# Optimization experiments

Hardware: AMD Instinct MI355X
Metric: run time of the kernel (lower is better)

## Reference

```python
import jax, jax.numpy as jnp
import numpy as np

N = 100000
E = 1000000
NODE_DIM = 128
EDGE_DIM = 32
HID = 64
HIER = 32
NUM_CLASS = 10
NUM_LAYERS = 3
BN_EPS = 1e-5


def setup_inputs() -> dict:
    key = jax.random.key(0)
    ks = jax.random.split(key, 16)
    s = 0.05
    return {
        "x": jax.random.normal(ks[0], (N, NODE_DIM), jnp.float32),
        "e": jax.random.normal(ks[1], (E, EDGE_DIM), jnp.float32),
        "c": jax.random.normal(ks[2], (N, HIER), jnp.float32),
        "w_node": jax.random.normal(ks[3], (NODE_DIM, HID), jnp.float32) * s,
        "b_node": jnp.zeros((HID,), jnp.float32),
        "w_edge": jax.random.normal(ks[4], (EDGE_DIM, HID), jnp.float32) * s,
        "b_edge": jnp.zeros((HID,), jnp.float32),
        "w_out1": jax.random.normal(ks[5], (HIER + HID, 2 * HID), jnp.float32) * s,
        "b_out1": jnp.zeros((2 * HID,), jnp.float32),
        "bn_gamma": jnp.ones((2 * HID,), jnp.float32),
        "bn_beta": jnp.zeros((2 * HID,), jnp.float32),
        "prelu_a": jnp.asarray(0.25, jnp.float32),
        "w_out2": jax.random.normal(ks[6], (2 * HID, NUM_CLASS), jnp.float32) * s,
        "b_out2": jnp.zeros((NUM_CLASS,), jnp.float32),
        "edge_index": jax.random.randint(ks[7], (2, E), 0, N, jnp.int64),
    }


def reference(x, e, c, w_node, b_node, w_edge, b_edge, w_out1, b_out1,
              bn_gamma, bn_beta, prelu_a, w_out2, b_out2, edge_index):
    n = x.shape[0]
    h = x @ w_node + b_node                      # [N, HID]
    eh = e @ w_edge + b_edge                     # [E, HID]
    src, dst = edge_index[0], edge_index[1]
    loop = jnp.arange(n)
    # add_self_loops + zero self-loop edge_attr (done inside each GCN layer,
    # identical every layer so hoisted)
    src_f = jnp.concatenate([src, loop])
    dst_f = jnp.concatenate([dst, loop])
    e_f = jnp.concatenate([eh, jnp.zeros((n, eh.shape[1]), eh.dtype)], axis=0)
    deg = jax.ops.segment_sum(jnp.ones(dst_f.shape, x.dtype), dst_f, num_segments=n)
    dinv = deg ** -0.5                           # deg >= 1 thanks to self loops
    norm = (dinv[src_f] * dinv[dst_f])[:, None]  # [E+N, 1]
    h_sum = h
    for _ in range(NUM_LAYERS):
        msg = norm * (h[src_f] + e_f)            # gather + edge compute
        h = jax.ops.segment_sum(msg, dst_f, num_segments=n)  # scatter-add
        h = jax.nn.leaky_relu(h, 0.2)
        h_sum = h_sum + h                        # sum over h_list
    z = jnp.concatenate([h_sum, c], axis=-1) @ w_out1 + b_out1
    # BatchNorm1d (training-mode batch statistics, biased variance)
    mu = z.mean(axis=0)
    var = z.var(axis=0)
    z = (z - mu) / jnp.sqrt(var + BN_EPS) * bn_gamma + bn_beta
    z = jnp.where(z > 0, z, prelu_a * z)         # PReLU (single param)
    return z @ w_out2 + b_out2
```

## Files before the change

### kernel.cpp

```cpp
#include <hip/hip_runtime.h>
#include <math.h>

#define N_NODES 100000
#define N_EDGES 1000000
#define HID     64
#define HIER    32
#define NDIM    128
#define EDIM    32
#define K1      96
#define C1      128
#define NCLS    10
#define BN_EPS  1e-5f
#define SCAN_B  98
#define HTILES2 782
#define ZSTRIPS 6250

typedef __attribute__((ext_vector_type(8))) short short8;
typedef __attribute__((ext_vector_type(4))) float f32x4;

__device__ __forceinline__ unsigned pk_bf16(float a, float b) {
    unsigned ua = __float_as_uint(a);
    ua = (ua + 0x7FFFu + ((ua >> 16) & 1u)) >> 16;
    unsigned ub = __float_as_uint(b);
    ub = (ub + 0x7FFFu + ((ub >> 16) & 1u)) & 0xFFFF0000u;
    return ua | ub;
}
__device__ __forceinline__ float bf_lo(unsigned g) { return __uint_as_float(g << 16); }
__device__ __forceinline__ float bf_hi(unsigned g) { return __uint_as_float(g & 0xFFFF0000u); }
__device__ __forceinline__ short8 as_s8(uint4 u) {
    union { uint4 u; short8 s; } c; c.u = u; return c.s;
}


__global__ void k_count(const int* __restrict__ ei, int* __restrict__ cnt) {
    int i = blockIdx.x * blockDim.x + threadIdx.x;
    if (i < N_EDGES) atomicAdd(&cnt[ei[N_EDGES + i]], 1);
}

__global__ void k_scan1(const int* __restrict__ cnt, int* __restrict__ offs,
                        float* __restrict__ dinv, int* __restrict__ bsum) {
    __shared__ int buf[2][1024];
    int t = threadIdx.x, b = blockIdx.x;
    int i = b * 1024 + t;
    int v = (i < N_NODES) ? cnt[i] : 0;
    buf[0][t] = v; __syncthreads();
    int pi = 0;
    for (int off = 1; off < 1024; off <<= 1) {
        int x = buf[pi][t];
        if (t >= off) x += buf[pi][t - off];
        buf[pi ^ 1][t] = x; __syncthreads(); pi ^= 1;
    }
    int incl = buf[pi][t];
    if (i < N_NODES) {
        offs[i] = incl - v;
        dinv[i] = rsqrtf((float)(v + 1));
    }
    if (t == 1023) bsum[b] = incl;
}

__global__ void k_scan2(int* __restrict__ bsum, int nb) {
    __shared__ int buf[2][1024];
    int t = threadIdx.x;
    int v = (t < nb) ? bsum[t] : 0;
    buf[0][t] = v; __syncthreads();
    int pi = 0;
    for (int off = 1; off < 1024; off <<= 1) {
        int x = buf[pi][t];
        if (t >= off) x += buf[pi][t - off];
        buf[pi ^ 1][t] = x; __syncthreads(); pi ^= 1;
    }
    int incl = buf[pi][t];
    if (t < nb) bsum[t] = incl - v;
}

__global__ void k_scan3(const int* __restrict__ bsum, int* __restrict__ offs) {
    int b = blockIdx.x;
    int i = b * 1024 + threadIdx.x;
    if (i < N_NODES) offs[i] += bsum[b];
    if (i == 0) offs[N_NODES] = N_EDGES;
}

__global__ void k_fill(const int* __restrict__ ei, const int* __restrict__ offs,
                       int* __restrict__ cursor, const float* __restrict__ dinv,
                       uint2* __restrict__ epk) {
    int i = blockIdx.x * blockDim.x + threadIdx.x;
    if (i >= N_EDGES) return;
    int s = ei[i], d = ei[N_EDGES + i];
    int pos = offs[d] + atomicAdd(&cursor[d], 1);
    unsigned nhi = pk_bf16(dinv[s], 0.f) << 16;
    epk[pos] = make_uint2((unsigned)i | ((unsigned)(s & 0xFFF) << 20),
                          nhi | (unsigned)(s >> 12));
}


__global__ __launch_bounds__(256) void k_conv(const float4* __restrict__ e4,
                                              uint4* __restrict__ eb4) {
    int i = blockIdx.x * 256 + threadIdx.x;
    float4 a = e4[(size_t)2 * i];
    float4 b = e4[(size_t)2 * i + 1];
    uint4 pk;
    pk.x = pk_bf16(a.x, a.y); pk.y = pk_bf16(a.z, a.w);
    pk.z = pk_bf16(b.x, b.y); pk.w = pk_bf16(b.z, b.w);
    eb4[i] = pk;
}

__global__ __launch_bounds__(256) void k_conv2(const float4* __restrict__ c4,
                                               uint2* __restrict__ cb2) {
    int i = blockIdx.x * 256 + threadIdx.x;
    if (i >= N_NODES * 8) return;
    float4 a = c4[i];
    cb2[i] = make_uint2(pk_bf16(a.x, a.y), pk_bf16(a.z, a.w));
}

__global__ __launch_bounds__(256) void k_wpack(const float* __restrict__ w1,
                                               uint4* __restrict__ bpkg) {
    int i = blockIdx.x * 256 + threadIdx.x;
    if (i >= 12 * C1) return;
    int g = i >> 7, n = i & 127;
    uint4 r;
    r.x = pk_bf16(w1[(8 * g + 0) * C1 + n], w1[(8 * g + 1) * C1 + n]);
    r.y = pk_bf16(w1[(8 * g + 2) * C1 + n], w1[(8 * g + 3) * C1 + n]);
    r.z = pk_bf16(w1[(8 * g + 4) * C1 + n], w1[(8 * g + 5) * C1 + n]);
    r.w = pk_bf16(w1[(8 * g + 6) * C1 + n], w1[(8 * g + 7) * C1 + n]);
    bpkg[i] = r;
}


__global__ __launch_bounds__(256) void k_agg3(const unsigned* __restrict__ ebfu,
                                              const uint2* __restrict__ epk,
                                              const int* __restrict__ offs,
                                              const float* __restrict__ dinv,
                                              float* __restrict__ agg,
                                              float* __restrict__ wsumv) {
    int v = (blockIdx.x * 256 + threadIdx.x) >> 4;
    if (v >= N_NODES) return;
    int q = threadIdx.x & 15;
    int start = offs[v], end = offs[v + 1];
    float ax = 0.f, ay = 0.f, wacc = 0.f;
    for (int i = start; i < end; i += 4) {
        int i1 = i + 1, i2 = i + 2, i3 = i + 3;
        uint2 p0 = epk[i];
        uint2 p1 = (i1 < end) ? epk[i1] : make_uint2(0u, 0u);
        uint2 p2 = (i2 < end) ? epk[i2] : make_uint2(0u, 0u);
        uint2 p3 = (i3 < end) ? epk[i3] : make_uint2(0u, 0u);
        float n0 = bf_hi(p0.y), n1 = bf_hi(p1.y);
        float n2 = bf_hi(p2.y), n3 = bf_hi(p3.y);
        unsigned g0 = ebfu[(size_t)(p0.x & 0xFFFFFu) * 16 + q];
        unsigned g1 = ebfu[(size_t)(p1.x & 0xFFFFFu) * 16 + q];
        unsigned g2 = ebfu[(size_t)(p2.x & 0xFFFFFu) * 16 + q];
        unsigned g3 = ebfu[(size_t)(p3.x & 0xFFFFFu) * 16 + q];
        ax += n0 * bf_lo(g0) + n1 * bf_lo(g1) + n2 * bf_lo(g2) + n3 * bf_lo(g3);
        ay += n0 * bf_hi(g0) + n1 * bf_hi(g1) + n2 * bf_hi(g2) + n3 * bf_hi(g3);
        wacc += n0 + n1 + n2 + n3;
    }
    float dv = dinv[v];
    *(float2*)&agg[(size_t)v * EDIM + q * 2] = make_float2(dv * ax, dv * ay);
    if (q == 0) wsumv[v] = dv * wacc;
}


__global__ __launch_bounds__(256) void k_h0t2(const float* __restrict__ x,
                                              const float* __restrict__ w,
                                              const float* __restrict__ bias,
                                              unsigned* __restrict__ hbf) {
    __shared__ __align__(16) unsigned wpk[NDIM * 36];
    __shared__ float xt[128 * 33];
    for (int i = threadIdx.x; i < NDIM * 32; i += 256) {
        int k = i >> 5, j = i & 31;
        wpk[k * 36 + j] = pk_bf16(w[k * HID + 2 * j], w[k * HID + 2 * j + 1]);
    }
    int tid = threadIdx.x;
    int lane = tid & 63, wave = tid >> 6;
    int lr = lane >> 3, lc = lane & 7;
    int rbase = wave * 32 + lr * 4;
    int cbase = lc * 8;
    float bA[8];
    #pragma unroll
    for (int j = 0; j < 8; ++j) bA[j] = bias[cbase + j];
    for (int tile = blockIdx.x; tile < HTILES2; tile += gridDim.x) {
        int row0 = tile * 128;
        float acc[4][8];
        #pragma unroll
        for (int i = 0; i < 4; ++i)
            #pragma unroll
            for (int j = 0; j < 8; ++j) acc[i][j] = 0.f;
        for (int ch = 0; ch < 4; ++ch) {
            __syncthreads();
            #pragma unroll
            for (int p = 0; p < 4; ++p) {
                int idx = p * 256 + tid;
                int row = idx >> 3, kq = idx & 7;
                int gk = ch * 32 + kq * 4;
                float4 v = make_float4(0.f, 0.f, 0.f, 0.f);
                int gr = row0 + row;
                if (gr < N_NODES) v = *(const float4*)&x[(size_t)gr * NDIM + gk];
                float* d = &xt[row * 33 + kq * 4];
                d[0] = v.x; d[1] = v.y; d[2] = v.z; d[3] = v.w;
            }
            __syncthreads();
            for (int k = 0; k < 32; ++k) {
                float u[4];
                #pragma unroll
                for (int i = 0; i < 4; ++i) u[i] = xt[(rbase + i) * 33 + k];
                uint4 wp = *(const uint4*)&wpk[(ch * 32 + k) * 36 + lc * 4];
                float wv[8];
                wv[0] = bf_lo(wp.x); wv[1] = bf_hi(wp.x);
                wv[2] = bf_lo(wp.y); wv[3] = bf_hi(wp.y);
                wv[4] = bf_lo(wp.z); wv[5] = bf_hi(wp.z);
                wv[6] = bf_lo(wp.w); wv[7] = bf_hi(wp.w);
                #pragma unroll
                for (int i = 0; i < 4; ++i)
                    #pragma unroll
                    for (int j = 0; j < 8; ++j) acc[i][j] += u[i] * wv[j];
            }
        }
        #pragma unroll
        for (int i = 0; i < 4; ++i) {
            int gr = row0 + rbase + i;
            if (gr < N_NODES) {
                uint4 pk;
                pk.x = pk_bf16(acc[i][0] + bA[0], acc[i][1] + bA[1]);
                pk.y = pk_bf16(acc[i][2] + bA[2], acc[i][3] + bA[3]);
                pk.z = pk_bf16(acc[i][4] + bA[4], acc[i][5] + bA[5]);
                pk.w = pk_bf16(acc[i][6] + bA[6], acc[i][7] + bA[7]);
                *(uint4*)&hbf[(size_t)gr * 32 + (cbase >> 1)] = pk;
            }
        }
    }
}


__global__ __launch_bounds__(256) void k_se(const float* __restrict__ agg,
                                            const float* __restrict__ wsumv,
                                            const float* __restrict__ we,
                                            const float* __restrict__ be,
                                            unsigned* __restrict__ sebf) {
    int lane = threadIdx.x & 63, wid = threadIdx.x >> 6;
    float wreg[EDIM];
    #pragma unroll
    for (int k = 0; k < EDIM; ++k) wreg[k] = we[k * HID + lane];
    float bl = be[lane];
    for (int v = blockIdx.x * 4 + wid; v < N_NODES; v += gridDim.x * 4) {
        const float4* ar = (const float4*)(agg + (size_t)v * EDIM);
        float acc = wsumv[v] * bl;
        #pragma unroll
        for (int k4 = 0; k4 < EDIM / 4; ++k4) {
            float4 av = ar[k4];
            int k = k4 * 4;
            acc += av.x * wreg[k + 0] + av.y * wreg[k + 1] +
                   av.z * wreg[k + 2] + av.w * wreg[k + 3];
        }
        float partner = __shfl_xor(acc, 1);
        if ((lane & 1) == 0)
            sebf[(size_t)v * 32 + (lane >> 1)] = pk_bf16(acc, partner);
    }
}


__device__ __forceinline__ int dec_src(uint2 p) {
    return (int)(((p.y & 0xFFFFu) << 12) | (p.x >> 20));
}

__global__ __launch_bounds__(256) void k_layer4(const unsigned* __restrict__ hold,
                                                const unsigned* __restrict__ sebf,
                                                const uint2* __restrict__ epk,
                                                const int* __restrict__ offs,
                                                const float* __restrict__ dinv,
                                                unsigned* __restrict__ hnew) {
    int v = (blockIdx.x * 256 + threadIdx.x) >> 4;
    if (v >= N_NODES) return;
    int q = threadIdx.x & 15;
    int start = offs[v], end = offs[v + 1];
    float dv = dinv[v];
    size_t vp = (size_t)v * 16 + q;
    uint2 hv = ((const uint2*)hold)[vp];
    float a0 = dv * bf_lo(hv.x), a1 = dv * bf_hi(hv.x);
    float a2 = dv * bf_lo(hv.y), a3 = dv * bf_hi(hv.y);
    for (int i = start; i < end; i += 8) {
        int idx[8]; float nn[8]; uint2 gg[8];
        #pragma unroll
        for (int u = 0; u < 8; ++u) {
            int ii = i + u;
            uint2 p = (ii < end) ? epk[ii] : make_uint2(0u, 0u);
            idx[u] = dec_src(p);
            nn[u]  = bf_hi(p.y);
        }
        #pragma unroll
        for (int u = 0; u < 8; ++u) gg[u] = ((const uint2*)hold)[(size_t)idx[u] * 16 + q];
        #pragma unroll
        for (int u = 0; u < 8; ++u) {
            a0 += nn[u] * bf_lo(gg[u].x); a1 += nn[u] * bf_hi(gg[u].x);
            a2 += nn[u] * bf_lo(gg[u].y); a3 += nn[u] * bf_hi(gg[u].y);
        }
    }
    uint2 sv = ((const uint2*)sebf)[vp];
    float r0 = bf_lo(sv.x) + dv * a0;
    float r1 = bf_hi(sv.x) + dv * a1;
    float r2 = bf_lo(sv.y) + dv * a2;
    float r3 = bf_hi(sv.y) + dv * a3;
    r0 = (r0 > 0.f) ? r0 : 0.2f * r0;
    r1 = (r1 > 0.f) ? r1 : 0.2f * r1;
    r2 = (r2 > 0.f) ? r2 : 0.2f * r2;
    r3 = (r3 > 0.f) ? r3 : 0.2f * r3;
    ((uint2*)hnew)[vp] = make_uint2(pk_bf16(r0, r1), pk_bf16(r2, r3));
}

__global__ __launch_bounds__(256) void k_layer4s(const unsigned* __restrict__ hold,
                                                 const unsigned* __restrict__ hb0,
                                                 const unsigned* __restrict__ hb1,
                                                 const unsigned* __restrict__ sebf,
                                                 const uint2* __restrict__ epk,
                                                 const int* __restrict__ offs,
                                                 const float* __restrict__ dinv,
                                                 unsigned* __restrict__ hnew,
                                                 unsigned* __restrict__ hsbf) {
    int v = (blockIdx.x * 256 + threadIdx.x) >> 4;
    if (v >= N_NODES) return;
    int q = threadIdx.x & 15;
    int start = offs[v], end = offs[v + 1];
    float dv = dinv[v];
    size_t vp = (size_t)v * 16 + q;
    uint2 hv = ((const uint2*)hold)[vp];
    float a0 = dv * bf_lo(hv.x), a1 = dv * bf_hi(hv.x);
    float a2 = dv * bf_lo(hv.y), a3 = dv * bf_hi(hv.y);
    for (int i = start; i < end; i += 8) {
        int idx[8]; float nn[8]; uint2 gg[8];
        #pragma unroll
        for (int u = 0; u < 8; ++u) {
            int ii = i + u;
            uint2 p = (ii < end) ? epk[ii] : make_uint2(0u, 0u);
            idx[u] = dec_src(p);
            nn[u]  = bf_hi(p.y);
        }
        #pragma unroll
        for (int u = 0; u < 8; ++u) gg[u] = ((const uint2*)hold)[(size_t)idx[u] * 16 + q];
        #pragma unroll
        for (int u = 0; u < 8; ++u) {
            a0 += nn[u] * bf_lo(gg[u].x); a1 += nn[u] * bf_hi(gg[u].x);
            a2 += nn[u] * bf_lo(gg[u].y); a3 += nn[u] * bf_hi(gg[u].y);
        }
    }
    uint2 sv = ((const uint2*)sebf)[vp];
    float r0 = bf_lo(sv.x) + dv * a0;
    float r1 = bf_hi(sv.x) + dv * a1;
    float r2 = bf_lo(sv.y) + dv * a2;
    float r3 = bf_hi(sv.y) + dv * a3;
    r0 = (r0 > 0.f) ? r0 : 0.2f * r0;
    r1 = (r1 > 0.f) ? r1 : 0.2f * r1;
    r2 = (r2 > 0.f) ? r2 : 0.2f * r2;
    r3 = (r3 > 0.f) ? r3 : 0.2f * r3;
    ((uint2*)hnew)[vp] = make_uint2(pk_bf16(r0, r1), pk_bf16(r2, r3));
    uint2 g0 = ((const uint2*)hb0)[vp];
    uint2 g1 = ((const uint2*)hb1)[vp];
    float s0 = r0 + bf_lo(g0.x) + bf_lo(g1.x) + bf_lo(hv.x);
    float s1 = r1 + bf_hi(g0.x) + bf_hi(g1.x) + bf_hi(hv.x);
    float s2 = r2 + bf_lo(g0.y) + bf_lo(g1.y) + bf_lo(hv.y);
    float s3 = r3 + bf_hi(g0.y) + bf_hi(g1.y) + bf_hi(hv.y);
    ((uint2*)hsbf)[vp] = make_uint2(pk_bf16(s0, s1), pk_bf16(s2, s3));
}


__global__ __launch_bounds__(256) void k_zmfma(const unsigned* __restrict__ hsbf,
                                               const unsigned* __restrict__ cbf,
                                               const uint4* __restrict__ bpkg,
                                               const float* __restrict__ b1,
                                               unsigned* __restrict__ zbf,
                                               float* __restrict__ stats) {
    __shared__ float red[2][4][C1];
    int tid = threadIdx.x;
    int wave = tid >> 6, lane = tid & 63;
    int l15 = lane & 15, lg = lane >> 4;
    int strip = blockIdx.x * 4 + wave;
    float sN[8], qN[8];
    #pragma unroll
    for (int j = 0; j < 8; ++j) { sN[j] = 0.f; qN[j] = 0.f; }
    if (strip < ZSTRIPS) {
        int row = strip * 16 + l15;
        short8 A0 = as_s8(*(const uint4*)&hsbf[(size_t)row * 32 + lg * 4]);
        short8 A1 = as_s8(*(const uint4*)&hsbf[(size_t)row * 32 + 16 + lg * 4]);
        short8 A2 = as_s8(*(const uint4*)&cbf[(size_t)row * 16 + lg * 4]);
        int rb = strip * 16 + lg * 4;
        #pragma unroll
        for (int ct = 0; ct < 8; ++ct) {
            int n = ct * 16 + l15;
            short8 B0 = as_s8(bpkg[lg * C1 + n]);
            short8 B1 = as_s8(bpkg[(4 + lg) * C1 + n]);
            short8 B2 = as_s8(bpkg[(8 + lg) * C1 + n]);
            f32x4 acc = {0.f, 0.f, 0.f, 0.f};
            acc = __builtin_amdgcn_mfma_f32_16x16x32_bf16(A0, B0, acc, 0, 0, 0);
            acc = __builtin_amdgcn_mfma_f32_16x16x32_bf16(A1, B1, acc, 0, 0, 0);
            acc = __builtin_amdgcn_mfma_f32_16x16x32_bf16(A2, B2, acc, 0, 0, 0);
            float bias = b1[n];
            #pragma unroll
            for (int i = 0; i < 4; ++i) {
                float zz = acc[i] + bias;
                sN[ct] += zz; qN[ct] += zz * zz;
                float pz = __shfl_xor(zz, 1);
                if ((l15 & 1) == 0)
                    zbf[(size_t)(rb + i) * 64 + (n >> 1)] = pk_bf16(zz, pz);
            }
        }
    }
    #pragma unroll
    for (int j = 0; j < 8; ++j) {
        sN[j] += __shfl_xor(sN[j], 16); sN[j] += __shfl_xor(sN[j], 32);
        qN[j] += __shfl_xor(qN[j], 16); qN[j] += __shfl_xor(qN[j], 32);
    }
    if (lane < 16) {
        #pragma unroll
        for (int ct = 0; ct < 8; ++ct) {
            red[0][wave][ct * 16 + lane] = sN[ct];
            red[1][wave][ct * 16 + lane] = qN[ct];
        }
    }
    __syncthreads();
    if (tid < C1) {
        atomicAdd(&stats[tid],
                  red[0][0][tid] + red[0][1][tid] + red[0][2][tid] + red[0][3][tid]);
        atomicAdd(&stats[C1 + tid],
                  red[1][0][tid] + red[1][1][tid] + red[1][2][tid] + red[1][3][tid]);
    }
}

__global__ void k_ab(const float* __restrict__ stats, const float* __restrict__ gamma,
                     const float* __restrict__ beta, float* __restrict__ ab) {
    int t = threadIdx.x;
    if (t < C1) {
        float mu = stats[t] / (float)N_NODES;
        float var = stats[C1 + t] / (float)N_NODES - mu * mu;
        float inv = rsqrtf(var + BN_EPS);
        float a = gamma[t] * inv;
        ab[t] = a;
        ab[C1 + t] = beta[t] - mu * a;
    }
}


__global__ __launch_bounds__(256) void k_out3(const unsigned* __restrict__ zbf,
                                              const float* __restrict__ ab,
                                              const float* __restrict__ pa,
                                              const float* __restrict__ w2,
                                              const float* __restrict__ b2,
                                              float* __restrict__ out) {
    int v = blockIdx.x * 256 + threadIdx.x;
    if (v >= N_NODES) return;
    float alpha = pa[0];
    float acc[NCLS];
    #pragma unroll
    for (int j = 0; j < NCLS; ++j) acc[j] = b2[j];
    const uint4* zr = (const uint4*)(zbf + (size_t)v * 64);
    #pragma unroll
    for (int pk4 = 0; pk4 < 16; ++pk4) {
        uint4 g = zr[pk4];
        unsigned gw[4] = {g.x, g.y, g.z, g.w};
        #pragma unroll
        for (int w = 0; w < 4; ++w) {
            int d0 = pk4 * 8 + w * 2;
            float p0 = bf_lo(gw[w]) * ab[d0]     + ab[C1 + d0];
            float p1 = bf_hi(gw[w]) * ab[d0 + 1] + ab[C1 + d0 + 1];
            p0 = (p0 > 0.f) ? p0 : alpha * p0;
            p1 = (p1 > 0.f) ? p1 : alpha * p1;
            #pragma unroll
            for (int j = 0; j < NCLS; ++j)
                acc[j] += p0 * w2[d0 * NCLS + j] + p1 * w2[(d0 + 1) * NCLS + j];
        }
    }
    #pragma unroll
    for (int j = 0; j < NCLS; ++j) out[(size_t)v * NCLS + j] = acc[j];
}


extern "C" void kernel_launch(void* const* d_in, const int* in_sizes, int n_in,
                              void* d_out, int out_size, void* d_ws, size_t ws_size,
                              hipStream_t stream) {
    const float* x      = (const float*)d_in[0];
    const float* e      = (const float*)d_in[1];
    const float* c      = (const float*)d_in[2];
    const float* w_node = (const float*)d_in[3];
    const float* b_node = (const float*)d_in[4];
    const float* w_edge = (const float*)d_in[5];
    const float* b_edge = (const float*)d_in[6];
    const float* w_out1 = (const float*)d_in[7];
    const float* b_out1 = (const float*)d_in[8];
    const float* gamma  = (const float*)d_in[9];
    const float* beta   = (const float*)d_in[10];
    const float* pa     = (const float*)d_in[11];
    const float* w_out2 = (const float*)d_in[12];
    const float* b_out2 = (const float*)d_in[13];
    const int*   ei     = (const int*)d_in[14];
    float* out = (float*)d_out;

    char* wsb = (char*)d_ws;
    ushort*   ebf  = (ushort*)wsb;
    unsigned* sebf = (unsigned*)wsb;
    unsigned* zbf  = (unsigned*)(wsb + 12800000);
    size_t off = (64000000 + 255) & ~(size_t)255;
    auto alloc = [&](size_t bytes) {
        void* p = wsb + off;
        off = (off + bytes + 255) & ~(size_t)255;
        return p;
    };
    int*      cnt      = (int*)alloc(4ull * N_NODES);
    int*      offs     = (int*)alloc(4ull * (N_NODES + 1));
    float*    dinv     = (float*)alloc(4ull * N_NODES);
    int*      bsum     = (int*)alloc(4ull * 128);
    uint2*    epk      = (uint2*)alloc(8ull * N_EDGES);
    float*    agg      = (float*)alloc(4ull * N_NODES * EDIM);
    float*    wsumv    = (float*)alloc(4ull * N_NODES);
    float*    stats    = (float*)alloc(4ull * 256);
    float*    ab       = (float*)alloc(4ull * 256);
    unsigned* hb0      = (unsigned*)alloc(4ull * N_NODES * 32);
    unsigned* hb1      = (unsigned*)alloc(4ull * N_NODES * 32);
    unsigned* hb2      = (unsigned*)alloc(4ull * N_NODES * 32);
    unsigned* hb3      = (unsigned*)alloc(4ull * N_NODES * 32);
    unsigned* cbf      = (unsigned*)alloc(4ull * N_NODES * 16);
    uint4*    bpkg     = (uint4*)alloc(16ull * 12 * C1);
    unsigned* hsbf     = (unsigned*)agg;

    hipMemsetAsync(cnt, 0, 4ull * N_NODES, stream);
    hipMemsetAsync(stats, 0, 4ull * 256, stream);

    k_count<<<(N_EDGES + 255) / 256, 256, 0, stream>>>(ei, cnt);
    k_scan1<<<SCAN_B, 1024, 0, stream>>>(cnt, offs, dinv, bsum);
    k_scan2<<<1, 1024, 0, stream>>>(bsum, SCAN_B);
    k_scan3<<<SCAN_B, 1024, 0, stream>>>(bsum, offs);
    hipMemsetAsync(cnt, 0, 4ull * N_NODES, stream);
    k_fill<<<(N_EDGES + 255) / 256, 256, 0, stream>>>(ei, offs, cnt, dinv, epk);

    k_wpack<<<6, 256, 0, stream>>>(w_out1, bpkg);
    k_conv<<<15625, 256, 0, stream>>>((const float4*)e, (uint4*)ebf);
    k_agg3<<<N_NODES * 16 / 256, 256, 0, stream>>>((const unsigned*)ebf, epk,
                                                   offs, dinv, agg, wsumv);

    k_se<<<1280, 256, 0, stream>>>(agg, wsumv, w_edge, b_edge, sebf);
    k_conv2<<<(N_NODES * 8 + 255) / 256, 256, 0, stream>>>((const float4*)c, (uint2*)cbf);
    k_h0t2<<<HTILES2, 256, 0, stream>>>(x, w_node, b_node, hb0);

    k_layer4<<<N_NODES * 16 / 256, 256, 0, stream>>>(hb0, sebf, epk, offs, dinv, hb1);
    k_layer4<<<N_NODES * 16 / 256, 256, 0, stream>>>(hb1, sebf, epk, offs, dinv, hb2);
    k_layer4s<<<N_NODES * 16 / 256, 256, 0, stream>>>(hb2, hb0, hb1, sebf, epk, offs,
                                                      dinv, hb3, hsbf);

    k_zmfma<<<(ZSTRIPS + 3) / 4, 256, 0, stream>>>(hsbf, cbf, bpkg, b_out1, zbf, stats);
    k_ab<<<1, 128, 0, stream>>>(stats, gamma, beta, ab);
    k_out3<<<(N_NODES + 255) / 256, 256, 0, stream>>>(zbf, ab, pa, w_out2, b_out2, out);
}
```

Before: 432.0 us.

## Use MFMA for node projection and fuse conversion and cursor-init kernels

The scalar LDS-tiled x @ w_node kernel becomes a bf16 MFMA kernel that converts x to bf16 in registers and reads pre-packed weights built in an extended k_wpack. The e and c bf16 conversion kernels are merged into one launch. The scan now initializes the fill cursor with the offsets, which removes a memset and a load of offs per edge in k_fill. Rounding x to bf16 before the matmul adds precision error, and the launch count drops.

```diff
diff --git a/kernel.cpp b/kernel.cpp
--- a/kernel.cpp
+++ b/kernel.cpp
@@ -12,8 +12,9 @@
 #define NCLS    10
 #define BN_EPS  1e-5f
 #define SCAN_B  98
-#define HTILES2 782
 #define ZSTRIPS 6250
+#define CONV_E_BLOCKS 15625
+#define CONV_C_BLOCKS 3125
 
 typedef __attribute__((ext_vector_type(8))) short short8;
 typedef __attribute__((ext_vector_type(4))) float f32x4;
@@ -73,56 +74,75 @@
     if (t < nb) bsum[t] = incl - v;
 }
 
-__global__ void k_scan3(const int* __restrict__ bsum, int* __restrict__ offs) {
+__global__ void k_scan3(const int* __restrict__ bsum, int* __restrict__ offs,
+                        int* __restrict__ cursor) {
     int b = blockIdx.x;
     int i = b * 1024 + threadIdx.x;
-    if (i < N_NODES) offs[i] += bsum[b];
+    if (i < N_NODES) {
+        int v = offs[i] + bsum[b];
+        offs[i] = v;
+        cursor[i] = v;
+    }
     if (i == 0) offs[N_NODES] = N_EDGES;
 }
 
-__global__ void k_fill(const int* __restrict__ ei, const int* __restrict__ offs,
-                       int* __restrict__ cursor, const float* __restrict__ dinv,
-                       uint2* __restrict__ epk) {
+__global__ void k_fill(const int* __restrict__ ei, int* __restrict__ cursor,
+                       const float* __restrict__ dinv, uint2* __restrict__ epk) {
     int i = blockIdx.x * blockDim.x + threadIdx.x;
     if (i >= N_EDGES) return;
     int s = ei[i], d = ei[N_EDGES + i];
-    int pos = offs[d] + atomicAdd(&cursor[d], 1);
+    int pos = atomicAdd(&cursor[d], 1);
     unsigned nhi = pk_bf16(dinv[s], 0.f) << 16;
     epk[pos] = make_uint2((unsigned)i | ((unsigned)(s & 0xFFF) << 20),
                           nhi | (unsigned)(s >> 12));
 }
 
 
-__global__ __launch_bounds__(256) void k_conv(const float4* __restrict__ e4,
-                                              uint4* __restrict__ eb4) {
-    int i = blockIdx.x * 256 + threadIdx.x;
-    float4 a = e4[(size_t)2 * i];
-    float4 b = e4[(size_t)2 * i + 1];
-    uint4 pk;
-    pk.x = pk_bf16(a.x, a.y); pk.y = pk_bf16(a.z, a.w);
-    pk.z = pk_bf16(b.x, b.y); pk.w = pk_bf16(b.z, b.w);
-    eb4[i] = pk;
-}
-
-__global__ __launch_bounds__(256) void k_conv2(const float4* __restrict__ c4,
+__global__ __launch_bounds__(256) void k_convm(const float4* __restrict__ e4,
+                                               uint4* __restrict__ eb4,
+                                               const float4* __restrict__ c4,
                                                uint2* __restrict__ cb2) {
-    int i = blockIdx.x * 256 + threadIdx.x;
-    if (i >= N_NODES * 8) return;
-    float4 a = c4[i];
-    cb2[i] = make_uint2(pk_bf16(a.x, a.y), pk_bf16(a.z, a.w));
-}
-
-__global__ __launch_bounds__(256) void k_wpack(const float* __restrict__ w1,
-                                               uint4* __restrict__ bpkg) {
-    int i = blockIdx.x * 256 + threadIdx.x;
-    if (i >= 12 * C1) return;
-    int g = i >> 7, n = i & 127;
-    uint4 r;
-    r.x = pk_bf16(w1[(8 * g + 0) * C1 + n], w1[(8 * g + 1) * C1 + n]);
-    r.y = pk_bf16(w1[(8 * g + 2) * C1 + n], w1[(8 * g + 3) * C1 + n]);
-    r.z = pk_bf16(w1[(8 * g + 4) * C1 + n], w1[(8 * g + 5) * C1 + n]);
-    r.w = pk_bf16(w1[(8 * g + 6) * C1 + n], w1[(8 * g + 7) * C1 + n]);
-    bpkg[i] = r;
+    int b = blockIdx.x;
+    if (b < CONV_E_BLOCKS) {
+        int i = b * 256 + threadIdx.x;
+        float4 a = e4[(size_t)2 * i];
+        float4 bb = e4[(size_t)2 * i + 1];
+        uint4 pk;
+        pk.x = pk_bf16(a.x, a.y); pk.y = pk_bf16(a.z, a.w);
+        pk.z = pk_bf16(bb.x, bb.y); pk.w = pk_bf16(bb.z, bb.w);
+        eb4[i] = pk;
+    } else {
+        int i = (b - CONV_E_BLOCKS) * 256 + threadIdx.x;
+        if (i < N_NODES * 8) {
+            float4 a = c4[i];
+            cb2[i] = make_uint2(pk_bf16(a.x, a.y), pk_bf16(a.z, a.w));
+        }
+    }
+}
+
+__global__ void k_wpack(const float* __restrict__ w1, const float* __restrict__ wn,
+                        uint4* __restrict__ bpkg, uint4* __restrict__ bpkn) {
+    for (int i = threadIdx.x; i < 12 * C1 + 16 * HID; i += 256) {
+        if (i < 12 * C1) {
+            int g = i >> 7, n = i & 127;
+            uint4 r;
+            r.x = pk_bf16(w1[(8 * g + 0) * C1 + n], w1[(8 * g + 1) * C1 + n]);
+            r.y = pk_bf16(w1[(8 * g + 2) * C1 + n], w1[(8 * g + 3) * C1 + n]);
+            r.z = pk_bf16(w1[(8 * g + 4) * C1 + n], w1[(8 * g + 5) * C1 + n]);
+            r.w = pk_bf16(w1[(8 * g + 6) * C1 + n], w1[(8 * g + 7) * C1 + n]);
+            bpkg[i] = r;
+        } else {
+            int j = i - 12 * C1;
+            int g = j >> 6, n = j & 63;
+            int kb = (g >> 2) * 32 + (g & 3) * 8;
+            uint4 r;
+            r.x = pk_bf16(wn[(kb + 0) * HID + n], wn[(kb + 1) * HID + n]);
+            r.y = pk_bf16(wn[(kb + 2) * HID + n], wn[(kb + 3) * HID + n]);
+            r.z = pk_bf16(wn[(kb + 4) * HID + n], wn[(kb + 5) * HID + n]);
+            r.w = pk_bf16(wn[(kb + 6) * HID + n], wn[(kb + 7) * HID + n]);
+            bpkn[j] = r;
+        }
+    }
 }
 
 
@@ -159,72 +179,43 @@
 }
 
 
-__global__ __launch_bounds__(256) void k_h0t2(const float* __restrict__ x,
-                                              const float* __restrict__ w,
-                                              const float* __restrict__ bias,
-                                              unsigned* __restrict__ hbf) {
-    __shared__ __align__(16) unsigned wpk[NDIM * 36];
-    __shared__ float xt[128 * 33];
-    for (int i = threadIdx.x; i < NDIM * 32; i += 256) {
-        int k = i >> 5, j = i & 31;
-        wpk[k * 36 + j] = pk_bf16(w[k * HID + 2 * j], w[k * HID + 2 * j + 1]);
-    }
+__global__ __launch_bounds__(256) void k_h0m(const float* __restrict__ x,
+                                             const uint4* __restrict__ bpkn,
+                                             const float* __restrict__ bias,
+                                             unsigned* __restrict__ hbf) {
     int tid = threadIdx.x;
-    int lane = tid & 63, wave = tid >> 6;
-    int lr = lane >> 3, lc = lane & 7;
-    int rbase = wave * 32 + lr * 4;
-    int cbase = lc * 8;
-    float bA[8];
-    #pragma unroll
-    for (int j = 0; j < 8; ++j) bA[j] = bias[cbase + j];
-    for (int tile = blockIdx.x; tile < HTILES2; tile += gridDim.x) {
-        int row0 = tile * 128;
-        float acc[4][8];
-        #pragma unroll
-        for (int i = 0; i < 4; ++i)
-            #pragma unroll
-            for (int j = 0; j < 8; ++j) acc[i][j] = 0.f;
-        for (int ch = 0; ch < 4; ++ch) {
-            __syncthreads();
-            #pragma unroll
-            for (int p = 0; p < 4; ++p) {
-                int idx = p * 256 + tid;
-                int row = idx >> 3, kq = idx & 7;
-                int gk = ch * 32 + kq * 4;
-                float4 v = make_float4(0.f, 0.f, 0.f, 0.f);
-                int gr = row0 + row;
-                if (gr < N_NODES) v = *(const float4*)&x[(size_t)gr * NDIM + gk];
-                float* d = &xt[row * 33 + kq * 4];
-                d[0] = v.x; d[1] = v.y; d[2] = v.z; d[3] = v.w;
-            }
-            __syncthreads();
-            for (int k = 0; k < 32; ++k) {
-                float u[4];
-                #pragma unroll
-                for (int i = 0; i < 4; ++i) u[i] = xt[(rbase + i) * 33 + k];
-                uint4 wp = *(const uint4*)&wpk[(ch * 32 + k) * 36 + lc * 4];
-                float wv[8];
-                wv[0] = bf_lo(wp.x); wv[1] = bf_hi(wp.x);
-                wv[2] = bf_lo(wp.y); wv[3] = bf_hi(wp.y);
-                wv[4] = bf_lo(wp.z); wv[5] = bf_hi(wp.z);
-                wv[6] = bf_lo(wp.w); wv[7] = bf_hi(wp.w);
-                #pragma unroll
-                for (int i = 0; i < 4; ++i)
-                    #pragma unroll
-                    for (int j = 0; j < 8; ++j) acc[i][j] += u[i] * wv[j];
-            }
-        }
+    int wave = tid >> 6, lane = tid & 63;
+    int l15 = lane & 15, lg = lane >> 4;
+    int strip = blockIdx.x * 4 + wave;
+    if (strip >= ZSTRIPS) return;
+    int row = strip * 16 + l15;
+    short8 A[4];
+    #pragma unroll
+    for (int kb = 0; kb < 4; ++kb) {
+        const float4* xp = (const float4*)&x[(size_t)row * NDIM + kb * 32 + lg * 8];
+        float4 a = xp[0], b = xp[1];
+        uint4 u;
+        u.x = pk_bf16(a.x, a.y); u.y = pk_bf16(a.z, a.w);
+        u.z = pk_bf16(b.x, b.y); u.w = pk_bf16(b.z, b.w);
+        A[kb] = as_s8(u);
+    }
+    int rb = strip * 16 + lg * 4;
+    #pragma unroll
+    for (int ct = 0; ct < 4; ++ct) {
+        int n = ct * 16 + l15;
+        f32x4 acc = {0.f, 0.f, 0.f, 0.f};
+        #pragma unroll
+        for (int kb = 0; kb < 4; ++kb) {
+            short8 B = as_s8(bpkn[(kb * 4 + lg) * HID + n]);
+            acc = __builtin_amdgcn_mfma_f32_16x16x32_bf16(A[kb], B, acc, 0, 0, 0);
+        }
+        float bn = bias[n];
         #pragma unroll
         for (int i = 0; i < 4; ++i) {
-            int gr = row0 + rbase + i;
-            if (gr < N_NODES) {
-                uint4 pk;
-                pk.x = pk_bf16(acc[i][0] + bA[0], acc[i][1] + bA[1]);
-                pk.y = pk_bf16(acc[i][2] + bA[2], acc[i][3] + bA[3]);
-                pk.z = pk_bf16(acc[i][4] + bA[4], acc[i][5] + bA[5]);
-                pk.w = pk_bf16(acc[i][6] + bA[6], acc[i][7] + bA[7]);
-                *(uint4*)&hbf[(size_t)gr * 32 + (cbase >> 1)] = pk;
-            }
+            float hv = acc[i] + bn;
+            float ph = __shfl_xor(hv, 1);
+            if ((l15 & 1) == 0)
+                hbf[(size_t)(rb + i) * 32 + (n >> 1)] = pk_bf16(hv, ph);
         }
     }
 }
@@ -515,6 +506,7 @@
     unsigned* hb3      = (unsigned*)alloc(4ull * N_NODES * 32);
     unsigned* cbf      = (unsigned*)alloc(4ull * N_NODES * 16);
     uint4*    bpkg     = (uint4*)alloc(16ull * 12 * C1);
+    uint4*    bpkn     = (uint4*)alloc(16ull * 16 * HID);
     unsigned* hsbf     = (unsigned*)agg;
 
     hipMemsetAsync(cnt, 0, 4ull * N_NODES, stream);
@@ -523,18 +515,17 @@
     k_count<<<(N_EDGES + 255) / 256, 256, 0, stream>>>(ei, cnt);
     k_scan1<<<SCAN_B, 1024, 0, stream>>>(cnt, offs, dinv, bsum);
     k_scan2<<<1, 1024, 0, stream>>>(bsum, SCAN_B);
-    k_scan3<<<SCAN_B, 1024, 0, stream>>>(bsum, offs);
-    hipMemsetAsync(cnt, 0, 4ull * N_NODES, stream);
-    k_fill<<<(N_EDGES + 255) / 256, 256, 0, stream>>>(ei, offs, cnt, dinv, epk);
-
-    k_wpack<<<6, 256, 0, stream>>>(w_out1, bpkg);
-    k_conv<<<15625, 256, 0, stream>>>((const float4*)e, (uint4*)ebf);
+    k_scan3<<<SCAN_B, 1024, 0, stream>>>(bsum, offs, cnt);
+    k_fill<<<(N_EDGES + 255) / 256, 256, 0, stream>>>(ei, cnt, dinv, epk);
+
+    k_wpack<<<1, 256, 0, stream>>>(w_out1, w_node, bpkg, bpkn);
+    k_convm<<<CONV_E_BLOCKS + CONV_C_BLOCKS, 256, 0, stream>>>(
+        (const float4*)e, (uint4*)ebf, (const float4*)c, (uint2*)cbf);
     k_agg3<<<N_NODES * 16 / 256, 256, 0, stream>>>((const unsigned*)ebf, epk,
                                                    offs, dinv, agg, wsumv);
 
     k_se<<<1280, 256, 0, stream>>>(agg, wsumv, w_edge, b_edge, sebf);
-    k_conv2<<<(N_NODES * 8 + 255) / 256, 256, 0, stream>>>((const float4*)c, (uint2*)cbf);
-    k_h0t2<<<HTILES2, 256, 0, stream>>>(x, w_node, b_node, hb0);
+    k_h0m<<<(ZSTRIPS + 3) / 4, 256, 0, stream>>>(x, bpkn, b_node, hb0);
 
     k_layer4<<<N_NODES * 16 / 256, 256, 0, stream>>>(hb0, sebf, epk, offs, dinv, hb1);
     k_layer4<<<N_NODES * 16 / 256, 256, 0, stream>>>(hb1, sebf, epk, offs, dinv, hb2);
```

New measurement: 413.2 us, median of 2. -4.4%, faster.
